# Kernel optimization log

Hardware: AMD Instinct MI355X
Metric: run time of the kernel (lower is better)

The kernel has to match this reference:

```python
import jax, jax.numpy as jnp
import numpy as np

N = 50000      # nodes
E = 1250000    # edges (avg degree 32)
D = 64         # in_channels == hidden_channels
L = 3          # num_layers
IMPROVED_FILL = 2.0  # GCNConv(improved=True) self-loop weight


def setup_inputs() -> dict:
    key = jax.random.key(0)
    ks = jax.random.split(key, 6)
    x = jax.random.normal(ks[0], (N, D), dtype=jnp.float32)
    edge_index = jax.random.randint(ks[1], (2, E), 0, N, dtype=jnp.int64)
    edge_weight = jax.random.uniform(ks[2], (E,), dtype=jnp.float32)
    Ws = jax.random.normal(ks[3], (L, D, D), dtype=jnp.float32) / np.sqrt(D).astype(np.float32)
    bs = jnp.zeros((L, D), dtype=jnp.float32)
    Wf = jax.random.normal(ks[4], (D, 1), dtype=jnp.float32) / np.sqrt(D).astype(np.float32)
    bf = jnp.zeros((1,), dtype=jnp.float32)
    return dict(x=x, edge_index=edge_index, edge_weight=edge_weight,
                Ws=Ws, bs=bs, Wf=Wf, bf=bf, prob=0)


def _gcn_norm(edge_index, edge_weight, n):
    # add self-loops with fill value 2.0 (improved=True)
    loop = jnp.arange(n, dtype=edge_index.dtype)
    row = jnp.concatenate([edge_index[0], loop])  # source nodes (x_j)
    col = jnp.concatenate([edge_index[1], loop])  # target nodes (aggregation)
    w = jnp.concatenate([edge_weight,
                         jnp.full((n,), IMPROVED_FILL, edge_weight.dtype)])
    deg = jax.ops.segment_sum(w, col, num_segments=n)
    dis = jnp.where(deg > 0, jax.lax.rsqrt(deg), 0.0)  # deg^{-1/2}, inf->0
    norm = dis[row] * w * dis[col]                      # [E+N]
    return row, col, norm


def reference(x, edge_index, edge_weight, Ws, bs, Wf, bf, prob):
    n = x.shape[0]
    # gcn_norm depends only on graph structure; compute once, reuse per layer
    row, col, norm = _gcn_norm(edge_index, edge_weight, n)
    for l in range(Ws.shape[0]):
        h = x @ Ws[l]                                  # [N, D] linear transform
        msg = h[row] * norm[:, None]                   # gather + per-edge scale
        agg = jax.ops.segment_sum(msg, col, num_segments=n)  # scatter-add
        x = jax.nn.relu(agg + bs[l])
    # F.dropout(x, p=prob) with prob=0 -> identity (inference)
    return x @ Wf + bf                                 # [N, 1]
```

## Files before the change

### kernel.cpp

```cpp
#include <hip/hip_runtime.h>
#include <hip/hip_bf16.h>

#define DCH 64
#define NB_CSR 256
#define MAXBINS 256

typedef __attribute__((ext_vector_type(8))) short bfrag;
typedef __attribute__((ext_vector_type(4))) float ffrag;

static __device__ __forceinline__ unsigned short f2bf(float f) {
    unsigned u = __float_as_uint(f);
    unsigned r = (u + 0x7fffu + ((u >> 16) & 1u)) >> 16;
    return (unsigned short)r;
}
static __device__ __forceinline__ float bf2f(unsigned short s) {
    return __uint_as_float(((unsigned)s) << 16);
}

__global__ __launch_bounds__(1024) void binc_k(const int* __restrict__ col,
                                               unsigned* __restrict__ blkcnt, int e) {
    __shared__ unsigned bins[MAXBINS];
    int B = blockIdx.x, tid = threadIdx.x;
    int chunk = (e + NB_CSR - 1) / NB_CSR;
    int beg = B * chunk, end = min(e, beg + chunk);
    if (tid < MAXBINS) bins[tid] = 0;
    __syncthreads();
    for (int i = beg + tid; i < end; i += 1024)
        atomicAdd(&bins[col[i] >> 8], 1u);
    __syncthreads();
    if (tid < MAXBINS) blkcnt[B * MAXBINS + tid] = bins[tid];
}

__global__ __launch_bounds__(64) void bincur1_k(const unsigned* __restrict__ blkcnt,
                                                unsigned* __restrict__ blkcur,
                                                unsigned* __restrict__ tot) {
    int j = blockIdx.x, lane = threadIdx.x;
    unsigned carry = 0;
#pragma unroll
    for (int c = 0; c < NB_CSR; c += 64) {
        unsigned v = blkcnt[(size_t)(c + lane) * MAXBINS + j];
        unsigned s = v;
#pragma unroll
        for (int off = 1; off < 64; off <<= 1) {
            unsigned t = __shfl_up(s, off);
            if (lane >= off) s += t;
        }
        blkcur[(size_t)(c + lane) * MAXBINS + j] = carry + s - v;
        carry += __shfl(s, 63);
    }
    if (lane == 0) tot[j] = carry;
}

__global__ __launch_bounds__(256) void bincur2_k(const unsigned* __restrict__ tot,
                                                 int* __restrict__ binbase,
                                                 int* __restrict__ ptr,
                                                 int nbins, int n, int e) {
    __shared__ int wtot[4];
    int tid = threadIdx.x, lane = tid & 63, w = tid >> 6;
    int v = (tid < nbins) ? (int)tot[tid] : 0;
    int s = v;
#pragma unroll
    for (int off = 1; off < 64; off <<= 1) {
        int t = __shfl_up(s, off);
        if (lane >= off) s += t;
    }
    if (lane == 63) wtot[w] = s;
    __syncthreads();
    if (tid == 0) {
        int r = 0;
#pragma unroll
        for (int k = 0; k < 4; ++k) { int t = wtot[k]; wtot[k] = r; r += t; }
    }
    __syncthreads();
    int excl = s - v + wtot[w];
    if (tid < nbins) binbase[tid] = excl;
    if (tid == 0) { binbase[nbins] = e; ptr[n] = e; }
}

__global__ __launch_bounds__(1024) void binfill_k(const int* __restrict__ row,
                                                  const int* __restrict__ col,
                                                  const float* __restrict__ ew,
                                                  const unsigned* __restrict__ blkcur,
                                                  const int* __restrict__ binbase,
                                                  uint2* __restrict__ rec, int e) {
    __shared__ unsigned cur[MAXBINS];
    int B = blockIdx.x, tid = threadIdx.x;
    int chunk = (e + NB_CSR - 1) / NB_CSR;
    int beg = B * chunk, end = min(e, beg + chunk);
    if (tid < MAXBINS) cur[tid] = blkcur[(size_t)B * MAXBINS + tid]
                                + (unsigned)binbase[tid];
    __syncthreads();
    for (int i = beg + tid; i < end; i += 1024) {
        int c = col[i];
        unsigned slot = atomicAdd(&cur[c >> 8], 1u);
        rec[slot] = make_uint2((unsigned)row[i] | ((unsigned)(c & 255) << 20),
                               __float_as_uint(ew[i]));
    }
}

__global__ __launch_bounds__(1024) void csr_k(const uint2* __restrict__ rec,
                                              const int* __restrict__ binbase,
                                              int* __restrict__ ptr,
                                              uint2* __restrict__ edg,
                                              float* __restrict__ dis, int n) {
    __shared__ unsigned ncnt[256];
    __shared__ unsigned nbase[256];
    __shared__ float degs[256];
    int b = blockIdx.x, tid = threadIdx.x;
    int beg = binbase[b], end = binbase[b + 1];
    int node0 = b << 8;
    int nn = min(256, n - node0);
    if (tid < 256) { ncnt[tid] = 0; degs[tid] = 0.f; }
    __syncthreads();
    for (int i = beg + tid; i < end; i += 1024) {
        uint2 r = rec[i];
        unsigned c8 = r.x >> 20;
        atomicAdd(&ncnt[c8], 1u);
        atomicAdd(&degs[c8], __uint_as_float(r.y));
    }
    __syncthreads();
    if (tid < 64) {
        unsigned carry = (unsigned)beg;
#pragma unroll
        for (int c = 0; c < 256; c += 64) {
            unsigned v = ncnt[c + tid];
            unsigned s = v;
#pragma unroll
            for (int off = 1; off < 64; off <<= 1) {
                unsigned t = __shfl_up(s, off);
                if (tid >= off) s += t;
            }
            nbase[c + tid] = carry + s - v;
            carry += __shfl(s, 63);
        }
    }
    __syncthreads();
    if (tid < nn) {
        ptr[node0 + tid] = (int)nbase[tid];
        dis[node0 + tid] = rsqrtf(degs[tid] + 2.0f);
    }
    if (tid < 256) ncnt[tid] = 0;
    __syncthreads();
    for (int i = beg + tid; i < end; i += 1024) {
        uint2 r = rec[i];
        unsigned c8 = r.x >> 20;
        unsigned pos = nbase[c8] + atomicAdd(&ncnt[c8], 1u);
        edg[pos] = make_uint2(r.x & 0xFFFFFu, r.y);
    }
}

__global__ __launch_bounds__(256) void normw_k(uint2* __restrict__ edg,
                                               const float* __restrict__ dis, int e) {
    int i = blockIdx.x * 256 + threadIdx.x;
    if (i >= e) return;
    uint2 ev = edg[i];
    ((unsigned*)edg)[2 * i + 1] =
        __float_as_uint(__uint_as_float(ev.y) * dis[ev.x]);
}

__global__ __launch_bounds__(256) void pack_k(const float* __restrict__ Ws,
                                              short* __restrict__ wpk, int L) {
    int ent = blockIdx.x * 256 + threadIdx.x;
    if (ent >= L * 512) return;
    int layer = ent >> 9;
    int r = ent & 511;
    int lane = r & 63;
    int st = r >> 6;
    int s = st >> 2, t = st & 3;
    int quad = lane >> 4;
    int ncol = t * 16 + (lane & 15);
    const float* W = Ws + (size_t)layer * DCH * DCH;
    union { short sh[8]; int4 v; } hi, lo;
#pragma unroll
    for (int j = 0; j < 8; ++j) {
        int k = s * 32 + quad * 8 + j;
        float w = W[k * DCH + ncol];
        unsigned short h = f2bf(w);
        hi.sh[j] = (short)h;
        lo.sh[j] = (short)f2bf(w - bf2f(h));
    }
    *(int4*)(wpk + ((size_t)(layer * 2 + 0) * 512 + r) * 8) = hi.v;
    *(int4*)(wpk + ((size_t)(layer * 2 + 1) * 512 + r) * 8) = lo.v;
}

__global__ __launch_bounds__(256) void gemm_k(const float* __restrict__ x,
                                              const short* __restrict__ wpk_layer,
                                              unsigned short* __restrict__ hb, int n_tiles) {
    __shared__ short Wl[2][512 * 8];
    {
        const int4* src = (const int4*)wpk_layer;
        int4* dst = (int4*)&Wl[0][0];
        for (int i = threadIdx.x; i < 1024; i += 256) dst[i] = src[i];
    }
    __syncthreads();
    int wave = threadIdx.x >> 6, lane = threadIdx.x & 63;
    int tile = blockIdx.x * 4 + wave;
    if (tile >= n_tiles) return;
    int m = lane & 15, quad = lane >> 4;
    int row = tile * 16 + m;

    float av[2][8];
    {
        const float4* p0 = (const float4*)(x + (size_t)row * DCH + quad * 8);
        const float4* p1 = (const float4*)(x + (size_t)row * DCH + 32 + quad * 8);
        float4 a0 = p0[0], a1 = p0[1], b0 = p1[0], b1 = p1[1];
        av[0][0] = a0.x; av[0][1] = a0.y; av[0][2] = a0.z; av[0][3] = a0.w;
        av[0][4] = a1.x; av[0][5] = a1.y; av[0][6] = a1.z; av[0][7] = a1.w;
        av[1][0] = b0.x; av[1][1] = b0.y; av[1][2] = b0.z; av[1][3] = b0.w;
        av[1][4] = b1.x; av[1][5] = b1.y; av[1][6] = b1.z; av[1][7] = b1.w;
    }
    bfrag ah[2], al[2];
#pragma unroll
    for (int s = 0; s < 2; ++s)
#pragma unroll
        for (int j = 0; j < 8; ++j) {
            unsigned short hbv = f2bf(av[s][j]);
            ah[s][j] = (short)hbv;
            al[s][j] = (short)f2bf(av[s][j] - bf2f(hbv));
        }

#pragma unroll
    for (int t = 0; t < 4; ++t) {
        ffrag acc = {0.f, 0.f, 0.f, 0.f};
#pragma unroll
        for (int s = 0; s < 2; ++s) {
            bfrag wh = *(bfrag*)&Wl[0][((s * 4 + t) * 64 + lane) * 8];
            bfrag wl = *(bfrag*)&Wl[1][((s * 4 + t) * 64 + lane) * 8];
            acc = __builtin_amdgcn_mfma_f32_16x16x32_bf16(ah[s], wh, acc, 0, 0, 0);
            acc = __builtin_amdgcn_mfma_f32_16x16x32_bf16(al[s], wh, acc, 0, 0, 0);
            acc = __builtin_amdgcn_mfma_f32_16x16x32_bf16(ah[s], wl, acc, 0, 0, 0);
        }
        int colc = t * 16 + m;
#pragma unroll
        for (int r = 0; r < 4; ++r)
            hb[(size_t)(tile * 16 + quad * 4 + r) * DCH + colc] = f2bf(acc[r]);
    }
}

static __device__ __forceinline__ void gather_node(int node, int lane, int pp, int eo,
                                                   float dis_c,
                                                   const int* __restrict__ ptr,
                                                   const uint2* __restrict__ edg,
                                                   const unsigned* __restrict__ hbf,
                                                   float a[4]) {
    a[0] = a[1] = a[2] = a[3] = 0.f;
    if (eo == 0) {
        uint2 sv = *(const uint2*)(hbf + (size_t)node * 32 + 2 * pp);
        float wsl = 2.0f * dis_c;
        a[0] = wsl * __uint_as_float(sv.x << 16);
        a[1] = wsl * __uint_as_float(sv.x & 0xffff0000u);
        a[2] = wsl * __uint_as_float(sv.y << 16);
        a[3] = wsl * __uint_as_float(sv.y & 0xffff0000u);
    }
    int beg = ptr[node], end = ptr[node + 1];
    for (int base = beg; base < end; base += 64) {
        int idx = base + lane;
        int rv = 0; float nv = 0.f;
        if (idx < end) {
            uint2 ev = edg[idx];
            rv = (int)ev.x;
            nv = __uint_as_float(ev.y);
        }
        int m = min(64, end - base);
        int steps = (((m + 3) >> 2) + 7) & ~7;
        for (int j0 = 0; j0 < steps; j0 += 8) {
            uint2 hv[8]; float nn[8];
#pragma unroll
            for (int q = 0; q < 8; ++q) {
                int eidx = 4 * (j0 + q) + eo;
                int r = __shfl(rv, eidx);
                nn[q] = __shfl(nv, eidx);
                hv[q] = *(const uint2*)(hbf + (size_t)r * 32 + 2 * pp);
            }
#pragma unroll
            for (int q = 0; q < 8; ++q) {
                a[0] += __uint_as_float(hv[q].x << 16) * nn[q];
                a[1] += __uint_as_float(hv[q].x & 0xffff0000u) * nn[q];
                a[2] += __uint_as_float(hv[q].y << 16) * nn[q];
                a[3] += __uint_as_float(hv[q].y & 0xffff0000u) * nn[q];
            }
        }
    }
#pragma unroll
    for (int j = 0; j < 4; ++j) {
        a[j] += __shfl_xor(a[j], 16);
        a[j] += __shfl_xor(a[j], 32);
    }
}

__global__ __launch_bounds__(256) void gg_k(const int* __restrict__ ptr,
                                            const uint2* __restrict__ edg,
                                            const float* __restrict__ dis,
                                            const unsigned* __restrict__ hbf,
                                            const float* __restrict__ b,
                                            const short* __restrict__ wpk_next,
                                            unsigned short* __restrict__ hb_out, int n) {
    __shared__ float xs[16][68];
    int w = threadIdx.x >> 6, lane = threadIdx.x & 63;
    int pp = lane & 15, eo = lane >> 4;
    int tile = blockIdx.x;
    float4 bv = ((const float4*)b)[pp];
#pragma unroll 1
    for (int i = 0; i < 4; ++i) {
        int node = tile * 16 + w * 4 + i;
        if (node < n) {
            float dis_c = dis[node];
            float a[4];
            gather_node(node, lane, pp, eo, dis_c, ptr, edg, hbf, a);
            if (eo == 0) {
                float4 o;
                o.x = fmaxf(dis_c * a[0] + bv.x, 0.f);
                o.y = fmaxf(dis_c * a[1] + bv.y, 0.f);
                o.z = fmaxf(dis_c * a[2] + bv.z, 0.f);
                o.w = fmaxf(dis_c * a[3] + bv.w, 0.f);
                *(float4*)&xs[w * 4 + i][4 * pp] = o;
            }
        }
    }
    __syncthreads();
    int m = lane & 15, quad = lane >> 4, t = w;
    bfrag ah[2], al[2];
#pragma unroll
    for (int s = 0; s < 2; ++s)
#pragma unroll
        for (int j = 0; j < 8; ++j) {
            float v = xs[m][s * 32 + quad * 8 + j];
            unsigned short hbv = f2bf(v);
            ah[s][j] = (short)hbv;
            al[s][j] = (short)f2bf(v - bf2f(hbv));
        }
    ffrag acc = {0.f, 0.f, 0.f, 0.f};
#pragma unroll
    for (int s = 0; s < 2; ++s) {
        bfrag wh = *(const bfrag*)(wpk_next + ((size_t)((s * 4 + t) * 64 + lane)) * 8);
        bfrag wl = *(const bfrag*)(wpk_next + ((size_t)(512 + (s * 4 + t) * 64 + lane)) * 8);
        acc = __builtin_amdgcn_mfma_f32_16x16x32_bf16(ah[s], wh, acc, 0, 0, 0);
        acc = __builtin_amdgcn_mfma_f32_16x16x32_bf16(al[s], wh, acc, 0, 0, 0);
        acc = __builtin_amdgcn_mfma_f32_16x16x32_bf16(ah[s], wl, acc, 0, 0, 0);
    }
    int colc = t * 16 + m;
#pragma unroll
    for (int r = 0; r < 4; ++r) {
        int orow = tile * 16 + quad * 4 + r;
        if (orow < n) hb_out[(size_t)orow * DCH + colc] = f2bf(acc[r]);
    }
}

__global__ __launch_bounds__(256) void gf_k(const int* __restrict__ ptr,
                                            const uint2* __restrict__ edg,
                                            const float* __restrict__ dis,
                                            const unsigned* __restrict__ hbf,
                                            const float* __restrict__ b,
                                            const float* __restrict__ Wf,
                                            const float* __restrict__ bf,
                                            float* __restrict__ out, int n) {
    int node = blockIdx.x * 4 + (threadIdx.x >> 6);
    int lane = threadIdx.x & 63;
    if (node >= n) return;
    int pp = lane & 15, eo = lane >> 4;
    float dis_c = dis[node];
    float a[4];
    gather_node(node, lane, pp, eo, dis_c, ptr, edg, hbf, a);
    float4 bv = ((const float4*)b)[pp];
    float4 wv = ((const float4*)Wf)[pp];
    float v = fmaxf(dis_c * a[0] + bv.x, 0.f) * wv.x
            + fmaxf(dis_c * a[1] + bv.y, 0.f) * wv.y
            + fmaxf(dis_c * a[2] + bv.z, 0.f) * wv.z
            + fmaxf(dis_c * a[3] + bv.w, 0.f) * wv.w;
#pragma unroll
    for (int off = 8; off > 0; off >>= 1) v += __shfl_xor(v, off);
    if (lane == 0) out[node] = v + bf[0];
}

extern "C" void kernel_launch(void* const* d_in, const int* in_sizes, int n_in,
                              void* d_out, int out_size, void* d_ws, size_t ws_size,
                              hipStream_t stream) {
    const float* x0 = (const float*)d_in[0];
    const int*   ei = (const int*)d_in[1];
    const float* ew = (const float*)d_in[2];
    const float* Ws = (const float*)d_in[3];
    const float* bs = (const float*)d_in[4];
    const float* Wf = (const float*)d_in[5];
    const float* bf = (const float*)d_in[6];

    const int n = in_sizes[0] / DCH;
    const int e = in_sizes[2];
    const int L = in_sizes[3] / (DCH * DCH);

    const int* row = ei;
    const int* col = ei + e;
    const int nbins = (n + 255) >> 8;

    size_t off = 0;
    auto alloc = [&](size_t bytes) {
        off = (off + 255) & ~(size_t)255;
        void* r = (char*)d_ws + off;
        off += bytes;
        return r;
    };
    int*      ptr     = (int*)     alloc((size_t)(n + 1) * 4);
    float*    dis     = (float*)   alloc((size_t)n * 4);
    short*    wpk     = (short*)   alloc((size_t)L * 2 * 512 * 8 * 2);
    uint2*    edg     = (uint2*)   alloc((size_t)e * 8);
    unsigned* blkcnt  = (unsigned*)alloc((size_t)NB_CSR * MAXBINS * 4);
    unsigned* blkcur  = (unsigned*)alloc((size_t)NB_CSR * MAXBINS * 4);
    unsigned* tot     = (unsigned*)alloc((size_t)MAXBINS * 4);
    int*      binbase = (int*)     alloc((size_t)(MAXBINS + 1) * 4);
    size_t szR = (size_t)e * 8;
    size_t szH = (size_t)2 * n * DCH * 2;
    unsigned char* regA = (unsigned char*)alloc(szR > szH ? szR : szH);
    uint2* rec = (uint2*)regA;
    unsigned short* hb_a = (unsigned short*)regA;
    unsigned short* hb_b = hb_a + (size_t)n * DCH;

    dim3 blk(256);
    const int n_tiles = (n + 15) / 16;

    binc_k   <<<dim3(NB_CSR), dim3(1024), 0, stream>>>(col, blkcnt, e);
    bincur1_k<<<dim3(nbins), dim3(64), 0, stream>>>(blkcnt, blkcur, tot);
    bincur2_k<<<dim3(1), blk, 0, stream>>>(tot, binbase, ptr, nbins, n, e);
    binfill_k<<<dim3(NB_CSR), dim3(1024), 0, stream>>>(row, col, ew, blkcur, binbase, rec, e);
    csr_k    <<<dim3(nbins), dim3(1024), 0, stream>>>(rec, binbase, ptr, edg, dis, n);
    normw_k  <<<dim3((e + 255) / 256), blk, 0, stream>>>(edg, dis, e);
    pack_k   <<<dim3((L * 512 + 255) / 256), blk, 0, stream>>>(Ws, wpk, L);

    const size_t wstride = (size_t)2 * 512 * 8;
    gemm_k<<<dim3((n_tiles + 3) / 4), blk, 0, stream>>>(x0, wpk, hb_a, n_tiles);
    gg_k  <<<dim3(n_tiles), blk, 0, stream>>>(ptr, edg, dis, (const unsigned*)hb_a,
                                              bs, wpk + wstride, hb_b, n);
    gg_k  <<<dim3(n_tiles), blk, 0, stream>>>(ptr, edg, dis, (const unsigned*)hb_b,
                                              bs + DCH, wpk + 2 * wstride, hb_a, n);
    gf_k  <<<dim3((n + 3) / 4), blk, 0, stream>>>(ptr, edg, dis, (const unsigned*)hb_a,
                                                  bs + 2 * DCH, Wf, bf, (float*)d_out, n);
}
```

Baseline: 209.0 us.

## Compute degrees in binning pass, fold source norm into binfill, prefetch edges in gg_k

Degree accumulation moves into the first binning kernel using global float atomics, and dis is computed in bincur1_k. The source-side normalisation is then applied while records are written in binfill_k, which removes the separate normw_k pass over all edges and the shared-memory degree loop in csr_k. gg_k now stages the tile's row pointers in shared memory and inlines the gather, prefetching the next node's first edge chunk while the current node is aggregated. Global atomics on deg add contention and make the summation order nondeterministic.

```diff
diff --git a/kernel.cpp b/kernel.cpp
--- a/kernel.cpp
+++ b/kernel.cpp
@@ -16,24 +16,37 @@
 static __device__ __forceinline__ float bf2f(unsigned short s) {
     return __uint_as_float(((unsigned)s) << 16);
 }
+static __device__ __forceinline__ float bf_lo(unsigned u) {
+    return __uint_as_float(u << 16);
+}
+static __device__ __forceinline__ float bf_hi(unsigned u) {
+    return __uint_as_float(u & 0xffff0000u);
+}
 
 __global__ __launch_bounds__(1024) void binc_k(const int* __restrict__ col,
-                                               unsigned* __restrict__ blkcnt, int e) {
+                                               const float* __restrict__ ew,
+                                               unsigned* __restrict__ blkcnt,
+                                               float* __restrict__ deg, int e) {
     __shared__ unsigned bins[MAXBINS];
     int B = blockIdx.x, tid = threadIdx.x;
     int chunk = (e + NB_CSR - 1) / NB_CSR;
     int beg = B * chunk, end = min(e, beg + chunk);
     if (tid < MAXBINS) bins[tid] = 0;
     __syncthreads();
-    for (int i = beg + tid; i < end; i += 1024)
-        atomicAdd(&bins[col[i] >> 8], 1u);
+    for (int i = beg + tid; i < end; i += 1024) {
+        int c = col[i];
+        atomicAdd(&bins[c >> 8], 1u);
+        atomicAdd(&deg[c], ew[i]);
+    }
     __syncthreads();
     if (tid < MAXBINS) blkcnt[B * MAXBINS + tid] = bins[tid];
 }
 
 __global__ __launch_bounds__(64) void bincur1_k(const unsigned* __restrict__ blkcnt,
                                                 unsigned* __restrict__ blkcur,
-                                                unsigned* __restrict__ tot) {
+                                                unsigned* __restrict__ tot,
+                                                const float* __restrict__ deg,
+                                                float* __restrict__ dis, int n) {
     int j = blockIdx.x, lane = threadIdx.x;
     unsigned carry = 0;
 #pragma unroll
@@ -49,6 +62,11 @@
         carry += __shfl(s, 63);
     }
     if (lane == 0) tot[j] = carry;
+#pragma unroll
+    for (int c = 0; c < 4; ++c) {
+        int idx = (j << 8) + c * 64 + lane;
+        if (idx < n) dis[idx] = rsqrtf(deg[idx] + 2.0f);
+    }
 }
 
 __global__ __launch_bounds__(256) void bincur2_k(const unsigned* __restrict__ tot,
@@ -80,6 +98,7 @@
 __global__ __launch_bounds__(1024) void binfill_k(const int* __restrict__ row,
                                                   const int* __restrict__ col,
                                                   const float* __restrict__ ew,
+                                                  const float* __restrict__ dis,
                                                   const unsigned* __restrict__ blkcur,
                                                   const int* __restrict__ binbase,
                                                   uint2* __restrict__ rec, int e) {
@@ -92,32 +111,27 @@
     __syncthreads();
     for (int i = beg + tid; i < end; i += 1024) {
         int c = col[i];
+        int r = row[i];
         unsigned slot = atomicAdd(&cur[c >> 8], 1u);
-        rec[slot] = make_uint2((unsigned)row[i] | ((unsigned)(c & 255) << 20),
-                               __float_as_uint(ew[i]));
+        rec[slot] = make_uint2((unsigned)r | ((unsigned)(c & 255) << 20),
+                               __float_as_uint(ew[i] * dis[r]));
     }
 }
 
 __global__ __launch_bounds__(1024) void csr_k(const uint2* __restrict__ rec,
                                               const int* __restrict__ binbase,
                                               int* __restrict__ ptr,
-                                              uint2* __restrict__ edg,
-                                              float* __restrict__ dis, int n) {
+                                              uint2* __restrict__ edg, int n) {
     __shared__ unsigned ncnt[256];
     __shared__ unsigned nbase[256];
-    __shared__ float degs[256];
     int b = blockIdx.x, tid = threadIdx.x;
     int beg = binbase[b], end = binbase[b + 1];
     int node0 = b << 8;
     int nn = min(256, n - node0);
-    if (tid < 256) { ncnt[tid] = 0; degs[tid] = 0.f; }
-    __syncthreads();
-    for (int i = beg + tid; i < end; i += 1024) {
-        uint2 r = rec[i];
-        unsigned c8 = r.x >> 20;
-        atomicAdd(&ncnt[c8], 1u);
-        atomicAdd(&degs[c8], __uint_as_float(r.y));
-    }
+    if (tid < 256) ncnt[tid] = 0;
+    __syncthreads();
+    for (int i = beg + tid; i < end; i += 1024)
+        atomicAdd(&ncnt[rec[i].x >> 20], 1u);
     __syncthreads();
     if (tid < 64) {
         unsigned carry = (unsigned)beg;
@@ -135,10 +149,7 @@
         }
     }
     __syncthreads();
-    if (tid < nn) {
-        ptr[node0 + tid] = (int)nbase[tid];
-        dis[node0 + tid] = rsqrtf(degs[tid] + 2.0f);
-    }
+    if (tid < nn) ptr[node0 + tid] = (int)nbase[tid];
     if (tid < 256) ncnt[tid] = 0;
     __syncthreads();
     for (int i = beg + tid; i < end; i += 1024) {
@@ -147,15 +158,6 @@
         unsigned pos = nbase[c8] + atomicAdd(&ncnt[c8], 1u);
         edg[pos] = make_uint2(r.x & 0xFFFFFu, r.y);
     }
-}
-
-__global__ __launch_bounds__(256) void normw_k(uint2* __restrict__ edg,
-                                               const float* __restrict__ dis, int e) {
-    int i = blockIdx.x * 256 + threadIdx.x;
-    if (i >= e) return;
-    uint2 ev = edg[i];
-    ((unsigned*)edg)[2 * i + 1] =
-        __float_as_uint(__uint_as_float(ev.y) * dis[ev.x]);
 }
 
 __global__ __launch_bounds__(256) void pack_k(const float* __restrict__ Ws,
@@ -247,10 +249,10 @@
     if (eo == 0) {
         uint2 sv = *(const uint2*)(hbf + (size_t)node * 32 + 2 * pp);
         float wsl = 2.0f * dis_c;
-        a[0] = wsl * __uint_as_float(sv.x << 16);
-        a[1] = wsl * __uint_as_float(sv.x & 0xffff0000u);
-        a[2] = wsl * __uint_as_float(sv.y << 16);
-        a[3] = wsl * __uint_as_float(sv.y & 0xffff0000u);
+        a[0] = wsl * bf_lo(sv.x);
+        a[1] = wsl * bf_hi(sv.x);
+        a[2] = wsl * bf_lo(sv.y);
+        a[3] = wsl * bf_hi(sv.y);
     }
     int beg = ptr[node], end = ptr[node + 1];
     for (int base = beg; base < end; base += 64) {
@@ -274,10 +276,10 @@
             }
 #pragma unroll
             for (int q = 0; q < 8; ++q) {
-                a[0] += __uint_as_float(hv[q].x << 16) * nn[q];
-                a[1] += __uint_as_float(hv[q].x & 0xffff0000u) * nn[q];
-                a[2] += __uint_as_float(hv[q].y << 16) * nn[q];
-                a[3] += __uint_as_float(hv[q].y & 0xffff0000u) * nn[q];
+                a[0] += bf_lo(hv[q].x) * nn[q];
+                a[1] += bf_hi(hv[q].x) * nn[q];
+                a[2] += bf_lo(hv[q].y) * nn[q];
+                a[3] += bf_hi(hv[q].y) * nn[q];
             }
         }
     }
@@ -296,25 +298,80 @@
                                             const short* __restrict__ wpk_next,
                                             unsigned short* __restrict__ hb_out, int n) {
     __shared__ float xs[16][68];
+    __shared__ int pt[17];
     int w = threadIdx.x >> 6, lane = threadIdx.x & 63;
     int pp = lane & 15, eo = lane >> 4;
     int tile = blockIdx.x;
+    if (threadIdx.x < 17)
+        pt[threadIdx.x] = ptr[min(tile * 16 + (int)threadIdx.x, n)];
+    __syncthreads();
     float4 bv = ((const float4*)b)[pp];
+    int s0 = w * 4;
+    uint2 evp;
+    {
+        int beg = pt[s0], end = pt[s0 + 1];
+        int idx = beg + lane;
+        evp = (idx < end) ? edg[idx] : make_uint2(0u, 0u);
+    }
 #pragma unroll 1
     for (int i = 0; i < 4; ++i) {
-        int node = tile * 16 + w * 4 + i;
-        if (node < n) {
-            float dis_c = dis[node];
-            float a[4];
-            gather_node(node, lane, pp, eo, dis_c, ptr, edg, hbf, a);
-            if (eo == 0) {
-                float4 o;
-                o.x = fmaxf(dis_c * a[0] + bv.x, 0.f);
-                o.y = fmaxf(dis_c * a[1] + bv.y, 0.f);
-                o.z = fmaxf(dis_c * a[2] + bv.z, 0.f);
-                o.w = fmaxf(dis_c * a[3] + bv.w, 0.f);
-                *(float4*)&xs[w * 4 + i][4 * pp] = o;
+        int slot = s0 + i;
+        int node = tile * 16 + slot;
+        int beg = pt[slot], end = pt[slot + 1];
+        uint2 ev0 = evp;
+        if (i < 3) {
+            int b2 = pt[slot + 1], e2 = pt[slot + 2];
+            int idx = b2 + lane;
+            evp = (idx < e2) ? edg[idx] : make_uint2(0u, 0u);
+        }
+        if (node >= n) continue;
+        float dis_c = dis[node];
+        float a0 = 0.f, a1 = 0.f, a2 = 0.f, a3 = 0.f;
+        if (eo == 0) {
+            uint2 sv = *(const uint2*)(hbf + (size_t)node * 32 + 2 * pp);
+            float wsl = 2.0f * dis_c;
+            a0 = wsl * bf_lo(sv.x); a1 = wsl * bf_hi(sv.x);
+            a2 = wsl * bf_lo(sv.y); a3 = wsl * bf_hi(sv.y);
+        }
+        for (int base = beg; base < end; base += 64) {
+            int rv; float nv;
+            if (base == beg) {
+                rv = (int)ev0.x; nv = __uint_as_float(ev0.y);
+            } else {
+                int idx = base + lane;
+                uint2 ev = (idx < end) ? edg[idx] : make_uint2(0u, 0u);
+                rv = (int)ev.x; nv = __uint_as_float(ev.y);
             }
+            int m = min(64, end - base);
+            int steps = (((m + 3) >> 2) + 7) & ~7;
+            for (int j0 = 0; j0 < steps; j0 += 8) {
+                uint2 hv[8]; float nn[8];
+#pragma unroll
+                for (int q = 0; q < 8; ++q) {
+                    int eidx = 4 * (j0 + q) + eo;
+                    int r = __shfl(rv, eidx);
+                    nn[q] = __shfl(nv, eidx);
+                    hv[q] = *(const uint2*)(hbf + (size_t)r * 32 + 2 * pp);
+                }
+#pragma unroll
+                for (int q = 0; q < 8; ++q) {
+                    float ww = nn[q];
+                    a0 += bf_lo(hv[q].x) * ww; a1 += bf_hi(hv[q].x) * ww;
+                    a2 += bf_lo(hv[q].y) * ww; a3 += bf_hi(hv[q].y) * ww;
+                }
+            }
+        }
+        a0 += __shfl_xor(a0, 16); a0 += __shfl_xor(a0, 32);
+        a1 += __shfl_xor(a1, 16); a1 += __shfl_xor(a1, 32);
+        a2 += __shfl_xor(a2, 16); a2 += __shfl_xor(a2, 32);
+        a3 += __shfl_xor(a3, 16); a3 += __shfl_xor(a3, 32);
+        if (eo == 0) {
+            float4 o;
+            o.x = fmaxf(dis_c * a0 + bv.x, 0.f);
+            o.y = fmaxf(dis_c * a1 + bv.y, 0.f);
+            o.z = fmaxf(dis_c * a2 + bv.z, 0.f);
+            o.w = fmaxf(dis_c * a3 + bv.w, 0.f);
+            *(float4*)&xs[slot][4 * pp] = o;
         }
     }
     __syncthreads();
@@ -400,6 +457,7 @@
     };
     int*      ptr     = (int*)     alloc((size_t)(n + 1) * 4);
     float*    dis     = (float*)   alloc((size_t)n * 4);
+    float*    deg     = (float*)   alloc((size_t)n * 4);
     short*    wpk     = (short*)   alloc((size_t)L * 2 * 512 * 8 * 2);
     uint2*    edg     = (uint2*)   alloc((size_t)e * 8);
     unsigned* blkcnt  = (unsigned*)alloc((size_t)NB_CSR * MAXBINS * 4);
@@ -416,12 +474,13 @@
     dim3 blk(256);
     const int n_tiles = (n + 15) / 16;
 
-    binc_k   <<<dim3(NB_CSR), dim3(1024), 0, stream>>>(col, blkcnt, e);
-    bincur1_k<<<dim3(nbins), dim3(64), 0, stream>>>(blkcnt, blkcur, tot);
+    hipMemsetAsync(deg, 0, (size_t)n * 4, stream);
+    binc_k   <<<dim3(NB_CSR), dim3(1024), 0, stream>>>(col, ew, blkcnt, deg, e);
+    bincur1_k<<<dim3(nbins), dim3(64), 0, stream>>>(blkcnt, blkcur, tot, deg, dis, n);
     bincur2_k<<<dim3(1), blk, 0, stream>>>(tot, binbase, ptr, nbins, n, e);
-    binfill_k<<<dim3(NB_CSR), dim3(1024), 0, stream>>>(row, col, ew, blkcur, binbase, rec, e);
-    csr_k    <<<dim3(nbins), dim3(1024), 0, stream>>>(rec, binbase, ptr, edg, dis, n);
-    normw_k  <<<dim3((e + 255) / 256), blk, 0, stream>>>(edg, dis, e);
+    binfill_k<<<dim3(NB_CSR), dim3(1024), 0, stream>>>(row, col, ew, dis, blkcur,
+                                                       binbase, rec, e);
+    csr_k    <<<dim3(nbins), dim3(1024), 0, stream>>>(rec, binbase, ptr, edg, n);
     pack_k   <<<dim3((L * 512 + 255) / 256), blk, 0, stream>>>(Ws, wpk, L);
 
     const size_t wstride = (size_t)2 * 512 * 8;
```

New measurement: 272.5 us. 1.3x slower.
